# Kernel optimization log

Measured on AMD Instinct MI355X. Metric: run time of the kernel, lower is better.

The kernel has to match this reference:

```python
import jax, jax.numpy as jnp
import numpy as np

N = 100000
D = 128


def segment_mean(x, idx, n):
    s = jax.ops.segment_sum(x, idx, num_segments=n)
    c = jax.ops.segment_sum(jnp.ones((idx.shape[0],), x.dtype), idx, num_segments=n)
    return s / jnp.maximum(c, 1.0)[:, None]


def setup_inputs() -> dict:
    key = jax.random.key(0)
    ks = jax.random.split(key, 10)
    scale = 1.0 / np.sqrt(D)
    return {
        "embedding": jax.random.normal(ks[0], (N, D), dtype=jnp.float32),
        "W_down": jax.random.normal(ks[1], (D, D), dtype=jnp.float32) * scale,
        "b_down": jnp.zeros((D,), dtype=jnp.float32),
        "W_gcn": jax.random.normal(ks[2], (D, D), dtype=jnp.float32) * scale,
        "b_gcn": jnp.zeros((D,), dtype=jnp.float32),
        "W_up": jax.random.normal(ks[3], (D, D), dtype=jnp.float32) * scale,
        "b_up": jnp.zeros((D,), dtype=jnp.float32),
        "down2up_path": jax.random.randint(ks[4], (2, 100000), 0, N),
        "same_level_edge_index": jax.random.randint(ks[5], (2, 600000), 0, N),
        "up2down_edge_index": jax.random.randint(ks[6], (2, 100000), 0, N),
    }


def _forward(embedding, W_down, b_down, W_gcn, b_gcn, W_up, b_up,
             down2up_path, same_level_edge_index, up2down_edge_index):
    # ---- Down2Up: aggregate children into parents (mean), transform, residual add ----
    src, dst = down2up_path[0], down2up_path[1]
    agg = segment_mean(embedding[src], dst, N)                     # [N, D]
    x = jax.nn.relu(embedding + agg @ W_down + b_down)

    # ---- Same-level GCNConv with self-loops and symmetric normalization ----
    s, d = same_level_edge_index[0], same_level_edge_index[1]
    h = x @ W_gcn                                                  # [N, D]
    deg = jax.ops.segment_sum(jnp.ones((s.shape[0],), h.dtype), d, num_segments=N) + 1.0
    dinv = jax.lax.rsqrt(deg)                                      # deg^{-1/2}
    norm = dinv[s] * dinv[d]                                       # [E]
    x = jax.ops.segment_sum(norm[:, None] * h[s], d, num_segments=N)
    x = x + h * (1.0 / deg)[:, None] + b_gcn                       # self-loop term

    # ---- Up2Down: propagate parents back down to children (mean), transform, residual ----
    src2, dst2 = up2down_edge_index[0], up2down_edge_index[1]
    agg2 = segment_mean(x[src2], dst2, N)
    return jax.nn.relu(x + agg2 @ W_up + b_up)


def reference(embedding, W_down, b_down, W_gcn, b_gcn, W_up, b_up,
              down2up_path, same_level_edge_index, up2down_edge_index):
    return _forward(embedding, W_down, b_down, W_gcn, b_gcn, W_up, b_up,
                    down2up_path, same_level_edge_index, up2down_edge_index)
```

## Files before the change

### kernel.cpp

```cpp
#include <hip/hip_runtime.h>
#include <cstdint>
#include <cstddef>

#define NNODES 100000
#define DIM 128

#define NB3   (3 * NNODES)
#define BSH   9
#define NBUCK ((NB3 + 511) >> 9)
#define EPB   2048

typedef unsigned short u16;
typedef uint32_t u32;
typedef __attribute__((ext_vector_type(8))) short v8s;
typedef __attribute__((ext_vector_type(4))) float v4f;

__device__ __forceinline__ float bf2f(u32 u) {
  union { u32 i; float f; } x; x.i = u << 16; return x.f;
}
__device__ __forceinline__ u16 f2bf(float f) {
  union { float f; u32 i; } x; x.f = f;
  u32 r = x.i + 0x7fffu + ((x.i >> 16) & 1u);
  return (u16)(r >> 16);
}
__device__ __forceinline__ u32 packsplit(float f) {
  u16 h = f2bf(f);
  float r = f - bf2f(h);
  u16 l = f2bf(r);
  return (u32)h | ((u32)l << 16);
}


__global__ __launch_bounds__(256) void bin_count(const int* __restrict__ d2u,
    const int* __restrict__ sle, const int* __restrict__ u2d,
    int E1, int E2, int E3, int* __restrict__ bcnt) {
  __shared__ int lc[NBUCK];
  const int tid = threadIdx.x;
  for (int i = tid; i < NBUCK; i += 256) lc[i] = 0;
  __syncthreads();
  const int Etot = E1 + E2 + E3;
  const int base = blockIdx.x * EPB;
#pragma unroll
  for (int k = 0; k < EPB; k += 256) {
    int e = base + k + tid;
    if (e < Etot) {
      int idx;
      if (e < E1)            idx = d2u[E1 + e];
      else if (e < E1 + E2)  idx = NNODES + sle[E2 + (e - E1)];
      else                   idx = 2 * NNODES + u2d[E3 + (e - E1 - E2)];
      atomicAdd(&lc[idx >> BSH], 1);
    }
  }
  __syncthreads();
  for (int i = tid; i < NBUCK; i += 256)
    if (lc[i]) atomicAdd(&bcnt[i], lc[i]);
}

__global__ void bin_scan(const int* __restrict__ bcnt, int* __restrict__ brs,
                         int* __restrict__ bfill) {
  __shared__ int tmp[1024];
  const int tid = threadIdx.x;
  for (int i = tid; i < 1024; i += 256) tmp[i] = (i < NBUCK) ? bcnt[i] : 0;
  __syncthreads();
  for (int off = 1; off < 1024; off <<= 1) {
    int vals[4];
#pragma unroll
    for (int j = 0; j < 4; ++j) { int i = tid + j * 256; vals[j] = (i >= off) ? tmp[i - off] : 0; }
    __syncthreads();
#pragma unroll
    for (int j = 0; j < 4; ++j) { int i = tid + j * 256; tmp[i] += vals[j]; }
    __syncthreads();
  }
  for (int i = tid; i < NBUCK; i += 256) {
    int excl = tmp[i] - bcnt[i];
    brs[i] = excl;
    bfill[i] = excl;
  }
}

__global__ __launch_bounds__(256) void bin_fill(const int* __restrict__ d2u,
    const int* __restrict__ sle, const int* __restrict__ u2d,
    int E1, int E2, int E3, int* __restrict__ bfill, uint2* __restrict__ pairs) {
  __shared__ int lc[NBUCK];
  const int tid = threadIdx.x;
  for (int i = tid; i < NBUCK; i += 256) lc[i] = 0;
  __syncthreads();
  const int Etot = E1 + E2 + E3;
  const int base = blockIdx.x * EPB;
  int vidx[EPB / 256], vsrc[EPB / 256];
#pragma unroll
  for (int k = 0; k < EPB / 256; ++k) {
    int e = base + k * 256 + tid;
    int idx = -1, src = 0;
    if (e < Etot) {
      if (e < E1)            { idx = d2u[E1 + e];                          src = d2u[e]; }
      else if (e < E1 + E2)  { int q = e - E1;      idx = NNODES + sle[E2 + q];      src = sle[q]; }
      else                   { int q = e - E1 - E2; idx = 2 * NNODES + u2d[E3 + q];  src = u2d[q]; }
      atomicAdd(&lc[idx >> BSH], 1);
    }
    vidx[k] = idx; vsrc[k] = src;
  }
  __syncthreads();
  for (int i = tid; i < NBUCK; i += 256) {
    int c = lc[i];
    if (c) lc[i] = atomicAdd(&bfill[i], c);
  }
  __syncthreads();
#pragma unroll
  for (int k = 0; k < EPB / 256; ++k) {
    int idx = vidx[k];
    if (idx >= 0) {
      int pos = atomicAdd(&lc[idx >> BSH], 1);
      pairs[pos] = make_uint2((unsigned)idx, (unsigned)vsrc[k]);
    }
  }
}

__global__ __launch_bounds__(256) void bucket_build(const uint2* __restrict__ pairs,
    const int* __restrict__ brs, const int* __restrict__ bcnt,
    int* __restrict__ cnt, int* __restrict__ rs, float* __restrict__ rnorm,
    int* __restrict__ eidx) {
  __shared__ int c[512];
  __shared__ int cur[512];
  __shared__ int wsum[4];
  const int tid = threadIdx.x;
  const int b = blockIdx.x;
  for (int i = tid; i < 512; i += 256) c[i] = 0;
  __syncthreads();
  const int s = brs[b], m = bcnt[b];
  for (int k = tid; k < m; k += 256) {
    uint2 p = pairs[s + k];
    atomicAdd(&c[p.x & 511], 1);
  }
  __syncthreads();
  const int v0 = c[tid * 2], v1 = c[tid * 2 + 1];
  const int tsum = v0 + v1;
  const int lane = tid & 63, wid = tid >> 6;
  int x = tsum;
  for (int off = 1; off < 64; off <<= 1) {
    int y = __shfl_up(x, off, 64);
    if (lane >= off) x += y;
  }
  if (lane == 63) wsum[wid] = x;
  __syncthreads();
  int woff = 0;
  for (int w = 0; w < wid; ++w) woff += wsum[w];
  const int excl = woff + x - tsum;
  const int node0 = b << BSH;
  const int g0 = node0 + tid * 2, g1 = g0 + 1;
  const int r0 = s + excl, r1 = s + excl + v0;
  if (g0 < NB3) {
    cnt[g0] = v0; rs[g0] = r0; cur[tid * 2] = r0;
    if (g0 >= NNODES && g0 < 2 * NNODES) rnorm[g0 - NNODES] = rsqrtf((float)v0 + 1.0f);
  }
  if (g1 < NB3) {
    cnt[g1] = v1; rs[g1] = r1; cur[tid * 2 + 1] = r1;
    if (g1 >= NNODES && g1 < 2 * NNODES) rnorm[g1 - NNODES] = rsqrtf((float)v1 + 1.0f);
  }
  __syncthreads();
  for (int k = tid; k < m; k += 256) {
    uint2 p = pairs[s + k];
    int pos = atomicAdd(&cur[p.x & 511], 1);
    eidx[pos] = (int)p.y;
  }
}

__global__ void make_w_planes(const float* __restrict__ W0, const float* __restrict__ W1,
                              const float* __restrict__ W2,
                              u16* __restrict__ Whi, u16* __restrict__ Wlo,
                              int* __restrict__ bcnt) {
  int i = blockIdx.x * 256 + threadIdx.x;
  if (i < 1024) bcnt[i] = 0;
  if (i >= 3 * DIM * DIM) return;
  int j = i & 7, lane = (i >> 3) & 63, ct = (i >> 9) & 7, kk = (i >> 12) & 3, m = i >> 14;
  int lr = lane & 15, quad = lane >> 4;
  int c = ct * 16 + lr;
  int k = kk * 32 + quad * 8 + j;
  const float* W = (m == 0) ? W0 : ((m == 1) ? W1 : W2);
  u32 p = packsplit(W[k * DIM + c]);
  Whi[i] = (u16)(p & 0xffffu);
  Wlo[i] = (u16)(p >> 16);
}


__global__ void gather_gcn(const u16* __restrict__ g,
                           const int* __restrict__ rs, const int* __restrict__ cnt,
                           const int* __restrict__ eidx, const float* __restrict__ rnorm,
                           const float* __restrict__ bias, float* __restrict__ out, int n) {
  int gid = blockIdx.x * 256 + threadIdx.x;
  int i = gid >> 6;
  if (i >= n) return;
  int sub = gid & 63;
  int c = (sub & 31) << 2;
  int start = rs[i], m = cnt[i];
  float4 acc = {0.f, 0.f, 0.f, 0.f};
  if (sub < 32) {
    ushort4 pv = *(const ushort4*)(g + ((size_t)i << 7) + c);
    acc.x = bf2f(pv.x); acc.y = bf2f(pv.y);
    acc.z = bf2f(pv.z); acc.w = bf2f(pv.w);
  }
  int j = sub >> 5;
  for (; j + 2 < m; j += 4) {
    int s0 = eidx[start + j], s1 = eidx[start + j + 2];
    ushort4 p0 = *(const ushort4*)(g + ((size_t)s0 << 7) + c);
    ushort4 p1 = *(const ushort4*)(g + ((size_t)s1 << 7) + c);
    acc.x += bf2f(p0.x) + bf2f(p1.x);
    acc.y += bf2f(p0.y) + bf2f(p1.y);
    acc.z += bf2f(p0.z) + bf2f(p1.z);
    acc.w += bf2f(p0.w) + bf2f(p1.w);
  }
  if (j < m) {
    int s = eidx[start + j];
    ushort4 pv = *(const ushort4*)(g + ((size_t)s << 7) + c);
    acc.x += bf2f(pv.x); acc.y += bf2f(pv.y);
    acc.z += bf2f(pv.z); acc.w += bf2f(pv.w);
  }
  acc.x += __shfl_xor(acc.x, 32);
  acc.y += __shfl_xor(acc.y, 32);
  acc.z += __shfl_xor(acc.z, 32);
  acc.w += __shfl_xor(acc.w, 32);
  if (sub < 32) {
    float ri = rnorm[i];
    float4 bv = *(const float4*)(bias + c);
    float4 o;
    o.x = fmaf(ri, acc.x, bv.x);
    o.y = fmaf(ri, acc.y, bv.y);
    o.z = fmaf(ri, acc.z, bv.z);
    o.w = fmaf(ri, acc.w, bv.w);
    *(float4*)(out + (size_t)i * DIM + c) = o;
  }
}

__global__ __launch_bounds__(512) void fused_ab(
    const float* __restrict__ emb,
    const int* __restrict__ rs, const int* __restrict__ cnt, const int* __restrict__ eidx,
    const u16* __restrict__ Wdh, const u16* __restrict__ Wdl,
    const u16* __restrict__ Wgh, const u16* __restrict__ Wgl,
    const float* __restrict__ bd, const float* __restrict__ rnorm,
    u16* __restrict__ obf, int nrows)
{
  __shared__ u16 S[32768];
  u32* X = (u32*)(S + 16384);
  const int tid = threadIdx.x;
  const int wave = tid >> 6, lane = tid & 63;
  const int lr = lane & 15, quad = lane >> 4;
  const int rowbase = blockIdx.x * 128 + wave * 16;

  int arow = rowbase + lr;
  if (arow >= nrows) arow = nrows - 1;
  const int start = rs[arow], m = cnt[arow];

  float4 fa[4], fb[4];
#pragma unroll
  for (int kk = 0; kk < 4; ++kk) {
    fa[kk] = (float4){0.f, 0.f, 0.f, 0.f};
    fb[kk] = (float4){0.f, 0.f, 0.f, 0.f};
  }
  for (int j = 0; j < m; ++j) {
    int s = eidx[start + j];
    const float* rp = emb + (size_t)s * DIM + quad * 8;
#pragma unroll
    for (int kk = 0; kk < 4; ++kk) {
      float4 v0 = *(const float4*)(rp + kk * 32);
      float4 v1 = *(const float4*)(rp + kk * 32 + 4);
      fa[kk].x += v0.x; fa[kk].y += v0.y; fa[kk].z += v0.z; fa[kk].w += v0.w;
      fb[kk].x += v1.x; fb[kk].y += v1.y; fb[kk].z += v1.z; fb[kk].w += v1.w;
    }
  }
  const float inv = 1.0f / fmaxf((float)m, 1.0f);
  v8s afh[4], afl[4];
#pragma unroll
  for (int kk = 0; kk < 4; ++kk) {
    float vs[8] = {fa[kk].x, fa[kk].y, fa[kk].z, fa[kk].w,
                   fb[kk].x, fb[kk].y, fb[kk].z, fb[kk].w};
#pragma unroll
    for (int j = 0; j < 8; ++j) {
      u32 p = packsplit(vs[j] * inv);
      afh[kk][j] = (short)(p & 0xffffu);
      afl[kk][j] = (short)(p >> 16);
    }
  }

  {
    uint4* S4 = (uint4*)S;
    for (int i = tid; i < 2048; i += 512) {
      S4[i] = ((const uint4*)Wdh)[i];
      S4[2048 + i] = ((const uint4*)Wdl)[i];
    }
  }
  __syncthreads();

  v4f acc[8];
#pragma unroll
  for (int ct = 0; ct < 8; ++ct) acc[ct] = (v4f){0.f, 0.f, 0.f, 0.f};
#pragma unroll
  for (int kk = 0; kk < 4; ++kk) {
#pragma unroll
    for (int ct = 0; ct < 8; ++ct) {
      const int wo = ((kk * 8 + ct) << 9) + (lane << 3);
      v8s bh = *(const v8s*)(S + wo);
      v8s bl = *(const v8s*)(S + 16384 + wo);
      acc[ct] = __builtin_amdgcn_mfma_f32_16x16x32_bf16(afh[kk], bh, acc[ct], 0, 0, 0);
      acc[ct] = __builtin_amdgcn_mfma_f32_16x16x32_bf16(afh[kk], bl, acc[ct], 0, 0, 0);
      acc[ct] = __builtin_amdgcn_mfma_f32_16x16x32_bf16(afl[kk], bh, acc[ct], 0, 0, 0);
    }
  }
  __syncthreads();

  {
    uint4* S4 = (uint4*)S;
    for (int i = tid; i < 2048; i += 512)
      S4[i] = ((const uint4*)Wgh)[i];
  }

#pragma unroll
  for (int cl = 0; cl < 2; ++cl) {
#pragma unroll
    for (int rg = 0; rg < 4; ++rg) {
      int r = rowbase + quad * 4 + rg;
      int rc = (r < nrows) ? r : (nrows - 1);
      const int col = cl * 16 + lr;
      float v = acc[cl][rg] + bd[col] + emb[(size_t)rc * DIM + col];
      v = fmaxf(v, 0.f);
      int slot = ((rg << 1) | cl) * 64 + (quad << 4) + lr;
      slot ^= ((slot >> 6) & 7) << 2;
      X[wave * 512 + slot] = packsplit(v);
    }
  }
  __syncthreads();

  v4f acc2[8];
#pragma unroll
  for (int ct = 0; ct < 8; ++ct) acc2[ct] = (v4f){0.f, 0.f, 0.f, 0.f};
#pragma unroll
  for (int Q = 0; Q < 4; ++Q) {
    v8s agh, agl;
    {
      int s0 = ((lr & 3) * 2 + (quad >> 1)) * 64 + ((lr >> 2) << 4) + ((quad & 1) << 3);
      int s1 = s0 + 4;
      s0 ^= ((s0 >> 6) & 7) << 2;
      s1 ^= ((s1 >> 6) & 7) << 2;
      uint4 q0 = *(const uint4*)(X + wave * 512 + s0);
      uint4 q1 = *(const uint4*)(X + wave * 512 + s1);
      u32 u[8] = {q0.x, q0.y, q0.z, q0.w, q1.x, q1.y, q1.z, q1.w};
#pragma unroll
      for (int j = 0; j < 8; ++j) {
        agh[j] = (short)(u[j] & 0xffffu);
        agl[j] = (short)(u[j] >> 16);
      }
    }
#pragma unroll
    for (int ct = 0; ct < 8; ++ct) {
      const int wo = ((Q * 8 + ct) << 9) + (lane << 3);
      v8s bh = *(const v8s*)(S + wo);
      v8s bl = *(const v8s*)(Wgl + wo);
      acc2[ct] = __builtin_amdgcn_mfma_f32_16x16x32_bf16(agh, bh, acc2[ct], 0, 0, 0);
      acc2[ct] = __builtin_amdgcn_mfma_f32_16x16x32_bf16(agh, bl, acc2[ct], 0, 0, 0);
      acc2[ct] = __builtin_amdgcn_mfma_f32_16x16x32_bf16(agl, bh, acc2[ct], 0, 0, 0);
    }
    if (Q < 3) {
#pragma unroll
      for (int cl = 0; cl < 2; ++cl) {
        int ct = 2 * (Q + 1) + cl;
#pragma unroll
        for (int rg = 0; rg < 4; ++rg) {
          int r = rowbase + quad * 4 + rg;
          int rc = (r < nrows) ? r : (nrows - 1);
          const int col = ct * 16 + lr;
          float v = acc[ct][rg] + bd[col] + emb[(size_t)rc * DIM + col];
          v = fmaxf(v, 0.f);
          int slot = ((rg << 1) | cl) * 64 + (quad << 4) + lr;
          slot ^= ((slot >> 6) & 7) << 2;
          X[wave * 512 + slot] = packsplit(v);
        }
      }
    }
  }

  __syncthreads();

  const int lrow0 = wave * 16 + quad * 4;
#pragma unroll
  for (int rg = 0; rg < 4; ++rg) {
    int lrow = lrow0 + rg;
    int r = blockIdx.x * 128 + lrow;
    float sc = rnorm[(r < nrows) ? r : (nrows - 1)];
    const int swz = (lrow & 7) << 4;
#pragma unroll
    for (int ct = 0; ct < 8; ++ct) {
      const int col = ct * 16 + lr;
      S[(lrow << 7) + (col ^ swz)] = f2bf(acc2[ct][rg] * sc);
    }
  }
  __syncthreads();
  const int rowstart = blockIdx.x * 128;
  for (int idx = tid; idx < 2048; idx += 512) {
    int lrow = idx >> 4, c8 = (idx & 15) << 3;
    int r = rowstart + lrow;
    if (r < nrows) {
      uint4 v = *(const uint4*)&S[(lrow << 7) + (c8 ^ ((lrow & 7) << 4))];
      *(uint4*)(obf + ((size_t)r << 7) + c8) = v;
    }
  }
}

__global__ __launch_bounds__(512) void gather_gemm_c(
    const float* __restrict__ x,
    const int* __restrict__ rs, const int* __restrict__ cnt, const int* __restrict__ eidx,
    const u16* __restrict__ Wuh, const u16* __restrict__ Wul,
    const float* __restrict__ bias, float* __restrict__ outf, int nrows)
{
  __shared__ u16 W[2 * DIM * DIM];
  const int tid = threadIdx.x;
  const int wave = tid >> 6, lane = tid & 63;
  const int lr = lane & 15, quad = lane >> 4;
  const int rowbase = blockIdx.x * 128 + wave * 16;

  int arow = rowbase + lr;
  if (arow >= nrows) arow = nrows - 1;
  const int start = rs[arow], m = cnt[arow];

  float4 fa[4], fb[4];
#pragma unroll
  for (int kk = 0; kk < 4; ++kk) {
    fa[kk] = (float4){0.f, 0.f, 0.f, 0.f};
    fb[kk] = (float4){0.f, 0.f, 0.f, 0.f};
  }
  for (int j = 0; j < m; ++j) {
    int s = eidx[start + j];
    const float* rp = x + (size_t)s * DIM + quad * 8;
#pragma unroll
    for (int kk = 0; kk < 4; ++kk) {
      float4 v0 = *(const float4*)(rp + kk * 32);
      float4 v1 = *(const float4*)(rp + kk * 32 + 4);
      fa[kk].x += v0.x; fa[kk].y += v0.y; fa[kk].z += v0.z; fa[kk].w += v0.w;
      fb[kk].x += v1.x; fb[kk].y += v1.y; fb[kk].z += v1.z; fb[kk].w += v1.w;
    }
  }
  const float inv = 1.0f / fmaxf((float)m, 1.0f);
  v8s afh[4], afl[4];
#pragma unroll
  for (int kk = 0; kk < 4; ++kk) {
    float vs[8] = {fa[kk].x, fa[kk].y, fa[kk].z, fa[kk].w,
                   fb[kk].x, fb[kk].y, fb[kk].z, fb[kk].w};
#pragma unroll
    for (int j = 0; j < 8; ++j) {
      u32 p = packsplit(vs[j] * inv);
      afh[kk][j] = (short)(p & 0xffffu);
      afl[kk][j] = (short)(p >> 16);
    }
  }

  {
    uint4* W4 = (uint4*)W;
    for (int i = tid; i < 2048; i += 512) {
      W4[i] = ((const uint4*)Wuh)[i];
      W4[2048 + i] = ((const uint4*)Wul)[i];
    }
  }
  __syncthreads();

  v4f acc[8];
#pragma unroll
  for (int ct = 0; ct < 8; ++ct) acc[ct] = (v4f){0.f, 0.f, 0.f, 0.f};
#pragma unroll
  for (int kk = 0; kk < 4; ++kk) {
#pragma unroll
    for (int ct = 0; ct < 8; ++ct) {
      const int wo = ((kk * 8 + ct) << 9) + (lane << 3);
      v8s bh = *(const v8s*)(W + wo);
      v8s bl = *(const v8s*)(W + DIM * DIM + wo);
      acc[ct] = __builtin_amdgcn_mfma_f32_16x16x32_bf16(afh[kk], bh, acc[ct], 0, 0, 0);
      acc[ct] = __builtin_amdgcn_mfma_f32_16x16x32_bf16(afh[kk], bl, acc[ct], 0, 0, 0);
      acc[ct] = __builtin_amdgcn_mfma_f32_16x16x32_bf16(afl[kk], bh, acc[ct], 0, 0, 0);
    }
  }

#pragma unroll
  for (int ct = 0; ct < 8; ++ct) {
    const int col = ct * 16 + lr;
    float bv = bias[col];
#pragma unroll
    for (int rg = 0; rg < 4; ++rg) {
      int r = rowbase + quad * 4 + rg;
      if (r < nrows) {
        size_t off = (size_t)r * DIM + col;
        float v = acc[ct][rg] + bv + x[off];
        outf[off] = fmaxf(v, 0.f);
      }
    }
  }
}


extern "C" void kernel_launch(void* const* d_in, const int* in_sizes, int n_in,
                              void* d_out, int out_size, void* d_ws, size_t ws_size,
                              hipStream_t stream) {
  const float* emb = (const float*)d_in[0];
  const float* Wd  = (const float*)d_in[1];
  const float* bd  = (const float*)d_in[2];
  const float* Wg  = (const float*)d_in[3];
  const float* bg  = (const float*)d_in[4];
  const float* Wu  = (const float*)d_in[5];
  const float* bu  = (const float*)d_in[6];
  const int* d2u = (const int*)d_in[7];
  const int* sle = (const int*)d_in[8];
  const int* u2d = (const int*)d_in[9];
  const int E1 = in_sizes[7] / 2;
  const int E2 = in_sizes[8] / 2;
  const int E3 = in_sizes[9] / 2;
  const int Etot = E1 + E2 + E3;
  const int N  = NNODES;
  const size_t nd = (size_t)N * DIM;

  float* xb = (float*)d_ws;
  u16* Gbf  = (u16*)(xb + nd);
  int* cnt  = (int*)(Gbf + nd);
  int* bbuf = cnt + 3 * N;
  int* rs   = bbuf + 3 * 1024;
  int* eidx = rs + 3 * N;
  float* rnorm = (float*)(eidx + Etot);
  int* bsum = (int*)(rnorm + N);
  u16* Whi = (u16*)(bsum + 1024);
  u16* Wlo = Whi + 3 * DIM * DIM;
  uint2* pairs = (uint2*)(Wlo + 3 * DIM * DIM);
  int* bcnt  = bbuf;
  int* brs   = bbuf + 1024;
  int* bfill = bbuf + 2048;

  const int gemm_blocks = (N + 127) / 128;
  const int ngcn = (N * 64 + 255) / 256;
  const int nbin = (Etot + EPB - 1) / EPB;

  make_w_planes<<<(3 * DIM * DIM + 255) / 256, 256, 0, stream>>>(Wd, Wg, Wu, Whi, Wlo, bcnt);
  bin_count<<<nbin, 256, 0, stream>>>(d2u, sle, u2d, E1, E2, E3, bcnt);
  bin_scan<<<1, 256, 0, stream>>>(bcnt, brs, bfill);
  bin_fill<<<nbin, 256, 0, stream>>>(d2u, sle, u2d, E1, E2, E3, bfill, pairs);
  bucket_build<<<NBUCK, 256, 0, stream>>>(pairs, brs, bcnt, cnt, rs, rnorm, eidx);

  fused_ab<<<gemm_blocks, 512, 0, stream>>>(emb, rs, cnt, eidx,
                                            Whi, Wlo, Whi + DIM * DIM, Wlo + DIM * DIM,
                                            bd, rnorm, Gbf, N);

  gather_gcn<<<ngcn, 256, 0, stream>>>(Gbf, rs + N, cnt + N, eidx, rnorm, bg, xb, N);

  gather_gemm_c<<<gemm_blocks, 512, 0, stream>>>(xb, rs + 2 * N, cnt + 2 * N, eidx,
                                                 Whi + 2 * DIM * DIM, Wlo + 2 * DIM * DIM,
                                                 bu, (float*)d_out, N);
}
```

Measured before the change: 274.1 us.

## Drop bin_scan kernel and halve weight LDS footprint in GEMM kernels

```diff
diff --git a/kernel.cpp b/kernel.cpp
--- a/kernel.cpp
+++ b/kernel.cpp
@@ -56,32 +56,12 @@
     if (lc[i]) atomicAdd(&bcnt[i], lc[i]);
 }
 
-__global__ void bin_scan(const int* __restrict__ bcnt, int* __restrict__ brs,
-                         int* __restrict__ bfill) {
-  __shared__ int tmp[1024];
-  const int tid = threadIdx.x;
-  for (int i = tid; i < 1024; i += 256) tmp[i] = (i < NBUCK) ? bcnt[i] : 0;
-  __syncthreads();
-  for (int off = 1; off < 1024; off <<= 1) {
-    int vals[4];
-#pragma unroll
-    for (int j = 0; j < 4; ++j) { int i = tid + j * 256; vals[j] = (i >= off) ? tmp[i - off] : 0; }
-    __syncthreads();
-#pragma unroll
-    for (int j = 0; j < 4; ++j) { int i = tid + j * 256; tmp[i] += vals[j]; }
-    __syncthreads();
-  }
-  for (int i = tid; i < NBUCK; i += 256) {
-    int excl = tmp[i] - bcnt[i];
-    brs[i] = excl;
-    bfill[i] = excl;
-  }
-}
-
 __global__ __launch_bounds__(256) void bin_fill(const int* __restrict__ d2u,
     const int* __restrict__ sle, const int* __restrict__ u2d,
-    int E1, int E2, int E3, int* __restrict__ bfill, uint2* __restrict__ pairs) {
+    int E1, int E2, int E3, const int* __restrict__ bcnt,
+    int* __restrict__ gfill, uint2* __restrict__ pairs) {
   __shared__ int lc[NBUCK];
+  __shared__ int sc[1024];
   const int tid = threadIdx.x;
   for (int i = tid; i < NBUCK; i += 256) lc[i] = 0;
   __syncthreads();
@@ -101,9 +81,20 @@
     vidx[k] = idx; vsrc[k] = src;
   }
   __syncthreads();
+  for (int i = tid; i < 1024; i += 256) sc[i] = (i < NBUCK) ? bcnt[i] : 0;
+  __syncthreads();
+  for (int off = 1; off < 1024; off <<= 1) {
+    int vals[4];
+#pragma unroll
+    for (int j = 0; j < 4; ++j) { int i = tid + j * 256; vals[j] = (i >= off) ? sc[i - off] : 0; }
+    __syncthreads();
+#pragma unroll
+    for (int j = 0; j < 4; ++j) { int i = tid + j * 256; sc[i] += vals[j]; }
+    __syncthreads();
+  }
   for (int i = tid; i < NBUCK; i += 256) {
     int c = lc[i];
-    if (c) lc[i] = atomicAdd(&bfill[i], c);
+    if (c) lc[i] = (sc[i] - bcnt[i]) + atomicAdd(&gfill[i], c);
   }
   __syncthreads();
 #pragma unroll
@@ -117,7 +108,7 @@
 }
 
 __global__ __launch_bounds__(256) void bucket_build(const uint2* __restrict__ pairs,
-    const int* __restrict__ brs, const int* __restrict__ bcnt,
+    const int* __restrict__ bcnt,
     int* __restrict__ cnt, int* __restrict__ rs, float* __restrict__ rnorm,
     int* __restrict__ eidx) {
   __shared__ int c[512];
@@ -125,9 +116,15 @@
   __shared__ int wsum[4];
   const int tid = threadIdx.x;
   const int b = blockIdx.x;
+  int part = 0;
+  for (int i = tid; i < b; i += 256) part += bcnt[i];
+#pragma unroll
+  for (int o = 32; o > 0; o >>= 1) part += __shfl_down(part, o, 64);
+  if ((tid & 63) == 0) wsum[tid >> 6] = part;
   for (int i = tid; i < 512; i += 256) c[i] = 0;
   __syncthreads();
-  const int s = brs[b], m = bcnt[b];
+  const int s = wsum[0] + wsum[1] + wsum[2] + wsum[3];
+  const int m = bcnt[b];
   for (int k = tid; k < m; k += 256) {
     uint2 p = pairs[s + k];
     atomicAdd(&c[p.x & 511], 1);
@@ -168,9 +165,9 @@
 __global__ void make_w_planes(const float* __restrict__ W0, const float* __restrict__ W1,
                               const float* __restrict__ W2,
                               u16* __restrict__ Whi, u16* __restrict__ Wlo,
-                              int* __restrict__ bcnt) {
+                              int* __restrict__ bbuf) {
   int i = blockIdx.x * 256 + threadIdx.x;
-  if (i < 1024) bcnt[i] = 0;
+  if (i < 2048) bbuf[i] = 0;
   if (i >= 3 * DIM * DIM) return;
   int j = i & 7, lane = (i >> 3) & 63, ct = (i >> 9) & 7, kk = (i >> 12) & 3, m = i >> 14;
   int lr = lane & 15, quad = lane >> 4;
@@ -239,7 +236,7 @@
     const float* __restrict__ bd, const float* __restrict__ rnorm,
     u16* __restrict__ obf, int nrows)
 {
-  __shared__ u16 S[32768];
+  __shared__ u16 S[24576];
   u32* X = (u32*)(S + 16384);
   const int tid = threadIdx.x;
   const int wave = tid >> 6, lane = tid & 63;
@@ -283,10 +280,8 @@
 
   {
     uint4* S4 = (uint4*)S;
-    for (int i = tid; i < 2048; i += 512) {
+    for (int i = tid; i < 2048; i += 512)
       S4[i] = ((const uint4*)Wdh)[i];
-      S4[2048 + i] = ((const uint4*)Wdl)[i];
-    }
   }
   __syncthreads();
 
@@ -299,10 +294,25 @@
     for (int ct = 0; ct < 8; ++ct) {
       const int wo = ((kk * 8 + ct) << 9) + (lane << 3);
       v8s bh = *(const v8s*)(S + wo);
-      v8s bl = *(const v8s*)(S + 16384 + wo);
       acc[ct] = __builtin_amdgcn_mfma_f32_16x16x32_bf16(afh[kk], bh, acc[ct], 0, 0, 0);
+      acc[ct] = __builtin_amdgcn_mfma_f32_16x16x32_bf16(afl[kk], bh, acc[ct], 0, 0, 0);
+    }
+  }
+  __syncthreads();
+
+  {
+    uint4* S4 = (uint4*)S;
+    for (int i = tid; i < 2048; i += 512)
+      S4[i] = ((const uint4*)Wdl)[i];
+  }
+  __syncthreads();
+#pragma unroll
+  for (int kk = 0; kk < 4; ++kk) {
+#pragma unroll
+    for (int ct = 0; ct < 8; ++ct) {
+      const int wo = ((kk * 8 + ct) << 9) + (lane << 3);
+      v8s bl = *(const v8s*)(S + wo);
       acc[ct] = __builtin_amdgcn_mfma_f32_16x16x32_bf16(afh[kk], bl, acc[ct], 0, 0, 0);
-      acc[ct] = __builtin_amdgcn_mfma_f32_16x16x32_bf16(afl[kk], bh, acc[ct], 0, 0, 0);
     }
   }
   __syncthreads();
@@ -410,7 +420,7 @@
     const u16* __restrict__ Wuh, const u16* __restrict__ Wul,
     const float* __restrict__ bias, float* __restrict__ outf, int nrows)
 {
-  __shared__ u16 W[2 * DIM * DIM];
+  __shared__ u16 W[DIM * DIM];
   const int tid = threadIdx.x;
   const int wave = tid >> 6, lane = tid & 63;
   const int lr = lane & 15, quad = lane >> 4;
@@ -453,10 +463,8 @@
 
   {
     uint4* W4 = (uint4*)W;
-    for (int i = tid; i < 2048; i += 512) {
+    for (int i = tid; i < 2048; i += 512)
       W4[i] = ((const uint4*)Wuh)[i];
-      W4[2048 + i] = ((const uint4*)Wul)[i];
-    }
   }
   __syncthreads();
 
@@ -469,10 +477,25 @@
     for (int ct = 0; ct < 8; ++ct) {
       const int wo = ((kk * 8 + ct) << 9) + (lane << 3);
       v8s bh = *(const v8s*)(W + wo);
-      v8s bl = *(const v8s*)(W + DIM * DIM + wo);
       acc[ct] = __builtin_amdgcn_mfma_f32_16x16x32_bf16(afh[kk], bh, acc[ct], 0, 0, 0);
+      acc[ct] = __builtin_amdgcn_mfma_f32_16x16x32_bf16(afl[kk], bh, acc[ct], 0, 0, 0);
+    }
+  }
+  __syncthreads();
+
+  {
+    uint4* W4 = (uint4*)W;
+    for (int i = tid; i < 2048; i += 512)
+      W4[i] = ((const uint4*)Wul)[i];
+  }
+  __syncthreads();
+#pragma unroll
+  for (int kk = 0; kk < 4; ++kk) {
+#pragma unroll
+    for (int ct = 0; ct < 8; ++ct) {
+      const int wo = ((kk * 8 + ct) << 9) + (lane << 3);
+      v8s bl = *(const v8s*)(W + wo);
       acc[ct] = __builtin_amdgcn_mfma_f32_16x16x32_bf16(afh[kk], bl, acc[ct], 0, 0, 0);
-      acc[ct] = __builtin_amdgcn_mfma_f32_16x16x32_bf16(afl[kk], bh, acc[ct], 0, 0, 0);
     }
   }
 
@@ -525,18 +548,16 @@
   u16* Wlo = Whi + 3 * DIM * DIM;
   uint2* pairs = (uint2*)(Wlo + 3 * DIM * DIM);
   int* bcnt  = bbuf;
-  int* brs   = bbuf + 1024;
-  int* bfill = bbuf + 2048;
+  int* gfill = bbuf + 1024;
 
   const int gemm_blocks = (N + 127) / 128;
   const int ngcn = (N * 64 + 255) / 256;
   const int nbin = (Etot + EPB - 1) / EPB;
 
-  make_w_planes<<<(3 * DIM * DIM + 255) / 256, 256, 0, stream>>>(Wd, Wg, Wu, Whi, Wlo, bcnt);
+  make_w_planes<<<(3 * DIM * DIM + 255) / 256, 256, 0, stream>>>(Wd, Wg, Wu, Whi, Wlo, bbuf);
   bin_count<<<nbin, 256, 0, stream>>>(d2u, sle, u2d, E1, E2, E3, bcnt);
-  bin_scan<<<1, 256, 0, stream>>>(bcnt, brs, bfill);
-  bin_fill<<<nbin, 256, 0, stream>>>(d2u, sle, u2d, E1, E2, E3, bfill, pairs);
-  bucket_build<<<NBUCK, 256, 0, stream>>>(pairs, brs, bcnt, cnt, rs, rnorm, eidx);
+  bin_fill<<<nbin, 256, 0, stream>>>(d2u, sle, u2d, E1, E2, E3, bcnt, gfill, pairs);
+  bucket_build<<<NBUCK, 256, 0, stream>>>(pairs, bcnt, cnt, rs, rnorm, eidx);
 
   fused_ab<<<gemm_blocks, 512, 0, stream>>>(emb, rs, cnt, eidx,
                                             Whi, Wlo, Whi + DIM * DIM, Wlo + DIM * DIM,
```

Measured after the change: 276.0 us. Within noise of the previous version (+0.7%).
